# Kernel tuning notes

Hardware: AMD Instinct MI355X
Metric: run time of the kernel (lower is better)

## Reference

```python
import jax, jax.numpy as jnp
import numpy as np

VOCAB = 64
H = 64
B, L = 256, 2048


def setup_inputs() -> dict:
    key = jax.random.key(0)
    ks = jax.random.split(key, 12)
    s = 0.02
    return {
        "seq":   jax.random.randint(ks[0], (B, L), 0, VOCAB),
        "embed": jax.random.normal(ks[1], (VOCAB, H), jnp.float32) * s,
        "W1":    jax.random.normal(ks[2], (H, 2 * H), jnp.float32) * s,
        "b1":    jnp.zeros((2 * H,), jnp.float32),
        "W2":    jax.random.normal(ks[3], (2 * H, H), jnp.float32) * s,
        "b2":    jnp.zeros((H,), jnp.float32),
        "gamma": jnp.ones((H,), jnp.float32),
        "beta":  jnp.zeros((H,), jnp.float32),
        "Wr":    jax.random.normal(ks[4], (H, H), jnp.float32) * s,
        "br":    jnp.zeros((H,), jnp.float32),
        "Wo":    jax.random.normal(ks[5], (H, VOCAB), jnp.float32) * s,
        "bo":    jnp.zeros((VOCAB,), jnp.float32),
    }


def _layernorm(x, gamma, beta, eps=1e-5):
    mu = x.mean(-1, keepdims=True)
    var = ((x - mu) ** 2).mean(-1, keepdims=True)
    return (x - mu) * jax.lax.rsqrt(var + eps) * gamma + beta


def _encode(seq, embed, W1, b1, W2, b2, gamma, beta):
    h = embed[seq]                                   # [B, L, H]
    ff = jax.nn.relu(h @ W1 + b1) @ W2 + b2
    return _layernorm(h + ff, gamma, beta)


def _run_memory(hidden):
    # sequential energy-gated delta-rule update of fast-weight M [B,H,H]
    Bd, Ld, Hd = hidden.shape
    M0 = jnp.zeros((Bd, Hd, Hd), hidden.dtype)

    def step(carry, k):
        M, writes = carry
        v = k                                        # k == v == hidden[:, t]
        v_pred = jnp.einsum('bij,bj->bi', M, k)
        denom = (k * k).sum(-1, keepdims=True) + 1e-6
        delta_v = v - v_pred / denom
        dM = delta_v[:, :, None] * k[:, None, :]     # outer product [B,H,H]
        E_before = -0.5 * (M * M).sum((-2, -1))
        Mn = M + dM
        E_after = -0.5 * (Mn * Mn).sum((-2, -1))
        gate = E_after < E_before                    # [B] bool
        M = jnp.where(gate[:, None, None], Mn, M)
        writes = writes + gate.sum().astype(jnp.float32)
        return (M, writes), None

    keys = jnp.swapaxes(hidden[:, :-1, :], 0, 1)     # [L-1, B, H]
    (M, writes), _ = jax.lax.scan(step, (M0, jnp.float32(0.0)), keys)
    return M, writes


def reference(seq, embed, W1, b1, W2, b2, gamma, beta, Wr, br, Wo, bo):
    hidden = _encode(seq, embed, W1, b1, W2, b2, gamma, beta)
    Bd, Ld, Hd = hidden.shape
    M, writes = _run_memory(hidden)
    write_rate = writes / jnp.float32(Bd * (Ld - 1))
    query = hidden[:, -1, :]
    ctx = jnp.einsum('bij,bj->bi', M, query)
    logits = (ctx @ Wr + br) @ Wo + bo               # [B, VOCAB]
    return logits, write_rate
```

## Files before the change

kernel.cpp:

```cpp
#include <hip/hip_runtime.h>
#include <math.h>

#define VOCAB 64
#define H 64
#define BB 256
#define LL 2048

typedef float v2f __attribute__((ext_vector_type(2)));

__device__ __forceinline__ float wave_sum_dpp(float x) {
  int t;
  float r = x;
  t = __builtin_amdgcn_update_dpp(0, __float_as_int(r), 0x111, 0xf, 0xf, true); r += __int_as_float(t);
  t = __builtin_amdgcn_update_dpp(0, __float_as_int(r), 0x112, 0xf, 0xf, true); r += __int_as_float(t);
  t = __builtin_amdgcn_update_dpp(0, __float_as_int(r), 0x114, 0xf, 0xf, true); r += __int_as_float(t);
  t = __builtin_amdgcn_update_dpp(0, __float_as_int(r), 0x118, 0xf, 0xf, true); r += __int_as_float(t);
  t = __builtin_amdgcn_update_dpp(0, __float_as_int(r), 0x142, 0xf, 0xf, true); r += __int_as_float(t);
  t = __builtin_amdgcn_update_dpp(0, __float_as_int(r), 0x143, 0xf, 0xf, true); r += __int_as_float(t);
  return __int_as_float(__builtin_amdgcn_readlane(__float_as_int(r), 63));
}

__global__ __launch_bounds__(64, 1) void encode_kernel(
    const float* __restrict__ embed, const float* __restrict__ W1,
    const float* __restrict__ b1, const float* __restrict__ W2,
    const float* __restrict__ b2, const float* __restrict__ gamma,
    const float* __restrict__ beta, float* __restrict__ table,
    float* __restrict__ kkg) {
  const int c = blockIdx.x;
  const int j = threadIdx.x;
  __shared__ float hs[H];
  __shared__ float zs[2 * H];
  const float h = embed[c * H + j];
  hs[j] = h;
  __syncthreads();
  float z0 = b1[j], z1 = b1[j + H];
#pragma unroll 8
  for (int i = 0; i < H; ++i) {
    const float hi = hs[i];
    z0 = fmaf(hi, W1[i * 2 * H + j], z0);
    z1 = fmaf(hi, W1[i * 2 * H + j + H], z1);
  }
  z0 = fmaxf(z0, 0.f);
  z1 = fmaxf(z1, 0.f);
  zs[j] = z0;
  zs[j + H] = z1;
  __syncthreads();
  float ff = b2[j];
#pragma unroll 8
  for (int m = 0; m < 2 * H; ++m) ff = fmaf(zs[m], W2[m * H + j], ff);
  const float x = h + ff;
  const float mu = wave_sum_dpp(x) * (1.f / 64.f);
  const float d = x - mu;
  const float var = wave_sum_dpp(d * d) * (1.f / 64.f);
  const float y = d * (1.f / sqrtf(var + 1e-5f)) * gamma[j] + beta[j];
  table[c * H + j] = y;
  const float s2 = wave_sum_dpp(y * y);
  if (j == 0) kkg[c] = s2;
}

__global__ __launch_bounds__(64, 1) void scan_kernel(
    const int* __restrict__ seq, const float* __restrict__ table,
    const float* __restrict__ kkg, const float* __restrict__ Wr,
    const float* __restrict__ br, const float* __restrict__ Wo,
    const float* __restrict__ bo, float* __restrict__ out,
    float* __restrict__ counts) {
  const int b = blockIdx.x;
  const int lane = threadIdx.x;
  __shared__ float T[H * VOCAB];
  __shared__ float KK[VOCAB];
  __shared__ int toks[LL];
  __shared__ float xv[H];

  {
    const float4* src = (const float4*)table;
    float4* dst = (float4*)T;
#pragma unroll
    for (int q = 0; q < 16; ++q) dst[q * 64 + lane] = src[q * 64 + lane];
    KK[lane] = kkg[lane];
    const int4* ssrc = (const int4*)(seq + (long)b * LL);
    int4* sdst = (int4*)toks;
#pragma unroll
    for (int q = 0; q < 8; ++q) sdst[q * 64 + lane] = ssrc[q * 64 + lane];
  }
  __syncthreads();

  v2f M2[32];
#pragma unroll
  for (int r = 0; r < 32; ++r) M2[r] = (v2f){0.f, 0.f};
  float wcount = 0.f;

  int c = toks[0];
  float sc = T[c * H + lane];
  float kk = KK[c];
  v2f vpA = (v2f){0.f, 0.f}, vpB = (v2f){0.f, 0.f};

  for (int t = 0; t < LL - 1; ++t) {
    const int cn = toks[t + 1];
    const float4* kvp = (const float4*)(T + c * H);
    const float4* knp = (const float4*)(T + cn * H);
    const float scn = T[cn * H + lane];
    const float kkn = KK[cn];

    const float vp = (vpA.x + vpA.y) + (vpB.x + vpB.y);
    const float dv = sc - vp / (kk + 1e-6f);
    const float a = dv * (2.f * vp + dv * kk);
    const float s = wave_sum_dpp(a);
    const float dvg = s > 0.f ? dv : 0.f;
    wcount += s > 0.f ? 1.f : 0.f;
    const v2f dv2 = (v2f){dvg, dvg};

    v2f nA = (v2f){0.f, 0.f}, nB = (v2f){0.f, 0.f};
#pragma unroll
    for (int q = 0; q < 16; ++q) {
      const float4 kv4 = kvp[q];
      const float4 kn4 = knp[q];
      const v2f kva = (v2f){kv4.x, kv4.y}, kvb = (v2f){kv4.z, kv4.w};
      const v2f kna = (v2f){kn4.x, kn4.y}, knb = (v2f){kn4.z, kn4.w};
      M2[2 * q]     = __builtin_elementwise_fma(dv2, kva, M2[2 * q]);
      M2[2 * q + 1] = __builtin_elementwise_fma(dv2, kvb, M2[2 * q + 1]);
      nA = __builtin_elementwise_fma(M2[2 * q],     kna, nA);
      nB = __builtin_elementwise_fma(M2[2 * q + 1], knb, nB);
    }
    vpA = nA; vpB = nB;
    c = cn; sc = scn; kk = kkn;
  }

  xv[lane] = (vpA.x + vpA.y) + (vpB.x + vpB.y);
  __syncthreads();
  float t1 = br[lane];
#pragma unroll 8
  for (int i = 0; i < H; ++i) t1 = fmaf(xv[i], Wr[i * H + lane], t1);
  __syncthreads();
  xv[lane] = t1;
  __syncthreads();
  float lg = bo[lane];
#pragma unroll 8
  for (int m = 0; m < H; ++m) lg = fmaf(xv[m], Wo[m * H + lane], lg);
  out[(long)b * H + lane] = lg;
  if (lane == 0) counts[b] = wcount;
}

__global__ __launch_bounds__(256, 1) void finalize_kernel(const float* __restrict__ counts,
                                                          float* __restrict__ out) {
  const int lane = threadIdx.x;
  __shared__ float sbuf[BB];
  sbuf[lane] = counts[lane];
  __syncthreads();
  for (int off = BB / 2; off > 0; off >>= 1) {
    if (lane < off) sbuf[lane] += sbuf[lane + off];
    __syncthreads();
  }
  if (lane == 0) out[BB * H] = sbuf[0] / (float)(BB * (LL - 1));
}

extern "C" void kernel_launch(void* const* d_in, const int* in_sizes, int n_in,
                              void* d_out, int out_size, void* d_ws, size_t ws_size,
                              hipStream_t stream) {
  const int* seq      = (const int*)d_in[0];
  const float* embed  = (const float*)d_in[1];
  const float* W1     = (const float*)d_in[2];
  const float* b1     = (const float*)d_in[3];
  const float* W2     = (const float*)d_in[4];
  const float* b2     = (const float*)d_in[5];
  const float* gamma  = (const float*)d_in[6];
  const float* beta   = (const float*)d_in[7];
  const float* Wr     = (const float*)d_in[8];
  const float* br     = (const float*)d_in[9];
  const float* Wo     = (const float*)d_in[10];
  const float* bo     = (const float*)d_in[11];
  float* out = (float*)d_out;

  float* table  = (float*)d_ws;
  float* kkg    = table + VOCAB * H;
  float* counts = kkg + VOCAB;

  encode_kernel<<<VOCAB, H, 0, stream>>>(embed, W1, b1, W2, b2, gamma, beta, table, kkg);
  scan_kernel<<<BB, H, 0, stream>>>(seq, table, kkg, Wr, br, Wo, bo, out, counts);
  finalize_kernel<<<1, BB, 0, stream>>>(counts, out);
}
```

Baseline: 724.8 us.

## Software-pipeline LDS key-row loads into rotating register buffers in scan loop

The sequential scan now prefetches the next token's 64-float key row from LDS into one of three rotating float4 register buffers, one step ahead. The loop is unrolled three ways with a macro so the buffers rotate without copies, hiding LDS latency behind the FMA work of the current step. This costs about 192 extra VGPRs on top of the 64 already used for M, which raises register pressure and may cause spills.

Measured after the change: 676.8 us. 6.6% less time.

```diff
diff --git a/kernel.cpp b/kernel.cpp
--- a/kernel.cpp
+++ b/kernel.cpp
@@ -58,6 +58,40 @@
   if (j == 0) kkg[c] = s2;
 }
 
+#define STEP(T_IDX, RU, RD, RP)                                              \
+  {                                                                          \
+    const int cp = cnn;           \
+    const int tpre = ((T_IDX) + 3 < LL) ? (T_IDX) + 3 : LL - 1;              \
+    const int cin = toks[tpre];                                              \
+    const float scp = T[cp * H + lane];                                      \
+    const float kkp = KK[cp];                                                \
+    const float4* rp = (const float4*)(T + cp * H);                          \
+    _Pragma("unroll")                                                        \
+    for (int q = 0; q < 16; ++q) RP[q] = rp[q];                              \
+    const float vp = (vpA.x + vpA.y) + (vpB.x + vpB.y);                      \
+    const float dv = sc - vp / (kk + 1e-6f);                                 \
+    const float aa = dv * (2.f * vp + dv * kk);                              \
+    const float s = wave_sum_dpp(aa);                                        \
+    const float dvg = s > 0.f ? dv : 0.f;                                    \
+    wcount += s > 0.f ? 1.f : 0.f;                                           \
+    const v2f dv2 = (v2f){dvg, dvg};                                         \
+    v2f nA = (v2f){0.f, 0.f}, nB = (v2f){0.f, 0.f};                          \
+    _Pragma("unroll")                                                        \
+    for (int q = 0; q < 16; ++q) {                                           \
+      const float4 kv4 = RU[q];                                              \
+      const float4 kn4 = RD[q];                                              \
+      const v2f kva = (v2f){kv4.x, kv4.y}, kvb = (v2f){kv4.z, kv4.w};        \
+      const v2f kna = (v2f){kn4.x, kn4.y}, knb = (v2f){kn4.z, kn4.w};        \
+      M2[2 * q]     = __builtin_elementwise_fma(dv2, kva, M2[2 * q]);        \
+      M2[2 * q + 1] = __builtin_elementwise_fma(dv2, kvb, M2[2 * q + 1]);    \
+      nA = __builtin_elementwise_fma(M2[2 * q],     kna, nA);                \
+      nB = __builtin_elementwise_fma(M2[2 * q + 1], knb, nB);                \
+    }                                                                        \
+    vpA = nA; vpB = nB;                                                      \
+    cn = cnn; cnn = cin;                                                     \
+    sc = scn; kk = kkn; scn = scp; kkn = kkp;                                \
+  }
+
 __global__ __launch_bounds__(64, 1) void scan_kernel(
     const int* __restrict__ seq, const float* __restrict__ table,
     const float* __restrict__ kkg, const float* __restrict__ Wr,
@@ -89,41 +123,26 @@
   for (int r = 0; r < 32; ++r) M2[r] = (v2f){0.f, 0.f};
   float wcount = 0.f;
 
-  int c = toks[0];
-  float sc = T[c * H + lane];
-  float kk = KK[c];
+  float4 RA[16], RB[16], RC[16];
+  const int c0 = toks[0];
+  int cn = toks[1], cnn = toks[2];
+  float sc = T[c0 * H + lane], kk = KK[c0];
+  float scn = T[cn * H + lane], kkn = KK[cn];
+  {
+    const float4* r0 = (const float4*)(T + c0 * H);
+    const float4* r1 = (const float4*)(T + cn * H);
+#pragma unroll
+    for (int q = 0; q < 16; ++q) { RA[q] = r0[q]; RB[q] = r1[q]; }
+  }
   v2f vpA = (v2f){0.f, 0.f}, vpB = (v2f){0.f, 0.f};
 
-  for (int t = 0; t < LL - 1; ++t) {
-    const int cn = toks[t + 1];
-    const float4* kvp = (const float4*)(T + c * H);
-    const float4* knp = (const float4*)(T + cn * H);
-    const float scn = T[cn * H + lane];
-    const float kkn = KK[cn];
-
-    const float vp = (vpA.x + vpA.y) + (vpB.x + vpB.y);
-    const float dv = sc - vp / (kk + 1e-6f);
-    const float a = dv * (2.f * vp + dv * kk);
-    const float s = wave_sum_dpp(a);
-    const float dvg = s > 0.f ? dv : 0.f;
-    wcount += s > 0.f ? 1.f : 0.f;
-    const v2f dv2 = (v2f){dvg, dvg};
-
-    v2f nA = (v2f){0.f, 0.f}, nB = (v2f){0.f, 0.f};
-#pragma unroll
-    for (int q = 0; q < 16; ++q) {
-      const float4 kv4 = kvp[q];
-      const float4 kn4 = knp[q];
-      const v2f kva = (v2f){kv4.x, kv4.y}, kvb = (v2f){kv4.z, kv4.w};
-      const v2f kna = (v2f){kn4.x, kn4.y}, knb = (v2f){kn4.z, kn4.w};
-      M2[2 * q]     = __builtin_elementwise_fma(dv2, kva, M2[2 * q]);
-      M2[2 * q + 1] = __builtin_elementwise_fma(dv2, kvb, M2[2 * q + 1]);
-      nA = __builtin_elementwise_fma(M2[2 * q],     kna, nA);
-      nB = __builtin_elementwise_fma(M2[2 * q + 1], knb, nB);
-    }
-    vpA = nA; vpB = nB;
-    c = cn; sc = scn; kk = kkn;
+  int t = 0;
+  for (int it = 0; it < 682; ++it) {
+    STEP(t, RA, RB, RC); ++t;
+    STEP(t, RB, RC, RA); ++t;
+    STEP(t, RC, RA, RB); ++t;
   }
+  STEP(t, RA, RB, RC);
 
   xv[lane] = (vpA.x + vpA.y) + (vpB.x + vpB.y);
   __syncthreads();
```

## Process two batch rows per wave to interleave independent scan recurrences

Applied to the files above, without the earlier changes.

Each scan block now handles two batch sequences (b and b+128), interleaving their delta-rule updates and wave reductions to hide the latency of the serial per-step chain. Token lookups are prefetched one step further ahead. The grid is halved, so only half as many compute units are used and per-wave register pressure roughly doubles.

After: 1.385 ms. 91.0% more time.

```diff
diff --git a/kernel.cpp b/kernel.cpp
--- a/kernel.cpp
+++ b/kernel.cpp
@@ -64,12 +64,15 @@
     const float* __restrict__ br, const float* __restrict__ Wo,
     const float* __restrict__ bo, float* __restrict__ out,
     float* __restrict__ counts) {
-  const int b = blockIdx.x;
+  const int b0 = blockIdx.x;
+  const int b1 = blockIdx.x + (BB / 2);
   const int lane = threadIdx.x;
   __shared__ float T[H * VOCAB];
   __shared__ float KK[VOCAB];
-  __shared__ int toks[LL];
-  __shared__ float xv[H];
+  __shared__ int tok0[LL];
+  __shared__ int tok1[LL];
+  __shared__ float xv[2][H];
+  __shared__ float yv[2][H];
 
   {
     const float4* src = (const float4*)table;
@@ -77,67 +80,106 @@
 #pragma unroll
     for (int q = 0; q < 16; ++q) dst[q * 64 + lane] = src[q * 64 + lane];
     KK[lane] = kkg[lane];
-    const int4* ssrc = (const int4*)(seq + (long)b * LL);
-    int4* sdst = (int4*)toks;
-#pragma unroll
-    for (int q = 0; q < 8; ++q) sdst[q * 64 + lane] = ssrc[q * 64 + lane];
-  }
-  __syncthreads();
-
-  v2f M2[32];
-#pragma unroll
-  for (int r = 0; r < 32; ++r) M2[r] = (v2f){0.f, 0.f};
-  float wcount = 0.f;
-
-  int c = toks[0];
-  float sc = T[c * H + lane];
-  float kk = KK[c];
-  v2f vpA = (v2f){0.f, 0.f}, vpB = (v2f){0.f, 0.f};
+    const int4* s0 = (const int4*)(seq + (long)b0 * LL);
+    const int4* s1 = (const int4*)(seq + (long)b1 * LL);
+    int4* d0 = (int4*)tok0;
+    int4* d1 = (int4*)tok1;
+#pragma unroll
+    for (int q = 0; q < 8; ++q) {
+      d0[q * 64 + lane] = s0[q * 64 + lane];
+      d1[q * 64 + lane] = s1[q * 64 + lane];
+    }
+  }
+  __syncthreads();
+
+  v2f M0[32], M1[32];
+#pragma unroll
+  for (int r = 0; r < 32; ++r) { M0[r] = (v2f){0.f, 0.f}; M1[r] = (v2f){0.f, 0.f}; }
+  float wc0 = 0.f, wc1 = 0.f;
+
+  int c0 = tok0[0], cn0 = tok0[1];
+  int c1 = tok1[0], cn1 = tok1[1];
+  float sc0 = T[c0 * H + lane], kk0 = KK[c0];
+  float scn0 = T[cn0 * H + lane], kkn0 = KK[cn0];
+  float sc1 = T[c1 * H + lane], kk1 = KK[c1];
+  float scn1 = T[cn1 * H + lane], kkn1 = KK[cn1];
+  v2f vA0 = (v2f){0.f, 0.f}, vB0 = (v2f){0.f, 0.f};
+  v2f vA1 = (v2f){0.f, 0.f}, vB1 = (v2f){0.f, 0.f};
 
   for (int t = 0; t < LL - 1; ++t) {
-    const int cn = toks[t + 1];
-    const float4* kvp = (const float4*)(T + c * H);
-    const float4* knp = (const float4*)(T + cn * H);
-    const float scn = T[cn * H + lane];
-    const float kkn = KK[cn];
-
-    const float vp = (vpA.x + vpA.y) + (vpB.x + vpB.y);
-    const float dv = sc - vp / (kk + 1e-6f);
-    const float a = dv * (2.f * vp + dv * kk);
-    const float s = wave_sum_dpp(a);
-    const float dvg = s > 0.f ? dv : 0.f;
-    wcount += s > 0.f ? 1.f : 0.f;
-    const v2f dv2 = (v2f){dvg, dvg};
-
-    v2f nA = (v2f){0.f, 0.f}, nB = (v2f){0.f, 0.f};
+    const int tp = (t + 2 < LL) ? t + 2 : LL - 1;
+    const int cp0 = tok0[tp], cp1 = tok1[tp];
+    const float scp0 = T[cp0 * H + lane], kkp0 = KK[cp0];
+    const float scp1 = T[cp1 * H + lane], kkp1 = KK[cp1];
+    const float4* u0 = (const float4*)(T + c0 * H);
+    const float4* d0 = (const float4*)(T + cn0 * H);
+    const float4* u1 = (const float4*)(T + c1 * H);
+    const float4* d1 = (const float4*)(T + cn1 * H);
+
+    const float vp0 = (vA0.x + vA0.y) + (vB0.x + vB0.y);
+    const float vp1 = (vA1.x + vA1.y) + (vB1.x + vB1.y);
+    const float dv0 = sc0 - vp0 / (kk0 + 1e-6f);
+    const float dv1 = sc1 - vp1 / (kk1 + 1e-6f);
+    const float a0 = dv0 * (2.f * vp0 + dv0 * kk0);
+    const float a1 = dv1 * (2.f * vp1 + dv1 * kk1);
+    const float s0 = wave_sum_dpp(a0);
+    const float s1 = wave_sum_dpp(a1);
+    const float g0 = s0 > 0.f ? dv0 : 0.f;
+    const float g1 = s1 > 0.f ? dv1 : 0.f;
+    wc0 += s0 > 0.f ? 1.f : 0.f;
+    wc1 += s1 > 0.f ? 1.f : 0.f;
+    const v2f d20 = (v2f){g0, g0};
+    const v2f d21 = (v2f){g1, g1};
+
+    v2f nA0 = (v2f){0.f, 0.f}, nB0 = (v2f){0.f, 0.f};
+    v2f nA1 = (v2f){0.f, 0.f}, nB1 = (v2f){0.f, 0.f};
 #pragma unroll
     for (int q = 0; q < 16; ++q) {
-      const float4 kv4 = kvp[q];
-      const float4 kn4 = knp[q];
-      const v2f kva = (v2f){kv4.x, kv4.y}, kvb = (v2f){kv4.z, kv4.w};
-      const v2f kna = (v2f){kn4.x, kn4.y}, knb = (v2f){kn4.z, kn4.w};
-      M2[2 * q]     = __builtin_elementwise_fma(dv2, kva, M2[2 * q]);
-      M2[2 * q + 1] = __builtin_elementwise_fma(dv2, kvb, M2[2 * q + 1]);
-      nA = __builtin_elementwise_fma(M2[2 * q],     kna, nA);
-      nB = __builtin_elementwise_fma(M2[2 * q + 1], knb, nB);
+      const float4 kv0 = u0[q];
+      const float4 kn0 = d0[q];
+      const float4 kv1 = u1[q];
+      const float4 kn1 = d1[q];
+      const v2f kva0 = (v2f){kv0.x, kv0.y}, kvb0 = (v2f){kv0.z, kv0.w};
+      const v2f kna0 = (v2f){kn0.x, kn0.y}, knb0 = (v2f){kn0.z, kn0.w};
+      const v2f kva1 = (v2f){kv1.x, kv1.y}, kvb1 = (v2f){kv1.z, kv1.w};
+      const v2f kna1 = (v2f){kn1.x, kn1.y}, knb1 = (v2f){kn1.z, kn1.w};
+      M0[2 * q]     = __builtin_elementwise_fma(d20, kva0, M0[2 * q]);
+      M0[2 * q + 1] = __builtin_elementwise_fma(d20, kvb0, M0[2 * q + 1]);
+      nA0 = __builtin_elementwise_fma(M0[2 * q],     kna0, nA0);
+      nB0 = __builtin_elementwise_fma(M0[2 * q + 1], knb0, nB0);
+      M1[2 * q]     = __builtin_elementwise_fma(d21, kva1, M1[2 * q]);
+      M1[2 * q + 1] = __builtin_elementwise_fma(d21, kvb1, M1[2 * q + 1]);
+      nA1 = __builtin_elementwise_fma(M1[2 * q],     kna1, nA1);
+      nB1 = __builtin_elementwise_fma(M1[2 * q + 1], knb1, nB1);
     }
-    vpA = nA; vpB = nB;
-    c = cn; sc = scn; kk = kkn;
-  }
-
-  xv[lane] = (vpA.x + vpA.y) + (vpB.x + vpB.y);
-  __syncthreads();
-  float t1 = br[lane];
-#pragma unroll 8
-  for (int i = 0; i < H; ++i) t1 = fmaf(xv[i], Wr[i * H + lane], t1);
-  __syncthreads();
-  xv[lane] = t1;
-  __syncthreads();
-  float lg = bo[lane];
-#pragma unroll 8
-  for (int m = 0; m < H; ++m) lg = fmaf(xv[m], Wo[m * H + lane], lg);
-  out[(long)b * H + lane] = lg;
-  if (lane == 0) counts[b] = wcount;
+    vA0 = nA0; vB0 = nB0; vA1 = nA1; vB1 = nB1;
+    c0 = cn0; cn0 = cp0; sc0 = scn0; kk0 = kkn0; scn0 = scp0; kkn0 = kkp0;
+    c1 = cn1; cn1 = cp1; sc1 = scn1; kk1 = kkn1; scn1 = scp1; kkn1 = kkp1;
+  }
+
+  xv[0][lane] = (vA0.x + vA0.y) + (vB0.x + vB0.y);
+  xv[1][lane] = (vA1.x + vA1.y) + (vB1.x + vB1.y);
+  __syncthreads();
+  float t10 = br[lane], t11 = br[lane];
+#pragma unroll 8
+  for (int i = 0; i < H; ++i) {
+    const float w = Wr[i * H + lane];
+    t10 = fmaf(xv[0][i], w, t10);
+    t11 = fmaf(xv[1][i], w, t11);
+  }
+  yv[0][lane] = t10;
+  yv[1][lane] = t11;
+  __syncthreads();
+  float lg0 = bo[lane], lg1 = bo[lane];
+#pragma unroll 8
+  for (int m = 0; m < H; ++m) {
+    const float w = Wo[m * VOCAB + lane];
+    lg0 = fmaf(yv[0][m], w, lg0);
+    lg1 = fmaf(yv[1][m], w, lg1);
+  }
+  out[(long)b0 * H + lane] = lg0;
+  out[(long)b1 * H + lane] = lg1;
+  if (lane == 0) { counts[b0] = wc0; counts[b1] = wc1; }
 }
 
 __global__ __launch_bounds__(256, 1) void finalize_kernel(const float* __restrict__ counts,
@@ -175,6 +217,6 @@
   float* counts = kkg + VOCAB;
 
   encode_kernel<<<VOCAB, H, 0, stream>>>(embed, W1, b1, W2, b2, gamma, beta, table, kkg);
-  scan_kernel<<<BB, H, 0, stream>>>(seq, table, kkg, Wr, br, Wo, bo, out, counts);
+  scan_kernel<<<BB / 2, H, 0, stream>>>(seq, table, kkg, Wr, br, Wo, bo, out, counts);
   finalize_kernel<<<1, BB, 0, stream>>>(counts, out);
 }
```
